# Performance work log

Measured on AMD Instinct MI355X. Metric: run time of the kernel, lower is better.

## Reference

```python
import jax, jax.numpy as jnp
import numpy as np

TEMPERATURE = 0.5


def setup_inputs() -> dict:
    key = jax.random.key(0)
    k1, k2 = jax.random.split(key)
    N, D = 4096, 512
    emb_i = jax.random.normal(k1, (N, D), dtype=jnp.float32)
    emb_j = jax.random.normal(k2, (N, D), dtype=jnp.float32)
    return {"emb_i": emb_i, "emb_j": emb_j}


def reference(emb_i, emb_j):
    # L2-normalize each embedding row (F.normalize, dim=1)
    z_i = emb_i / jnp.linalg.norm(emb_i, axis=1, keepdims=True)
    z_j = emb_j / jnp.linalg.norm(emb_j, axis=1, keepdims=True)
    reps = jnp.concatenate([z_i, z_j], axis=0)  # [2N, D]
    N = emb_i.shape[0]
    M = 2 * N
    # cosine similarity of normalized vectors == dot product -> [2N, 2N]
    sim = jnp.einsum('id,jd->ij', reps, reps) / TEMPERATURE
    # denominator: sum_k!=i exp(sim[i,k]); original multiplies by one-hot complement
    exp_sim = jnp.exp(sim)
    denom = jnp.sum(exp_sim, axis=1) - jnp.diagonal(exp_sim)  # [2N]
    log_denom = jnp.log(denom)
    # positive pairs: (k, k+N) and (k+N, k)
    idx = jnp.arange(N)
    pos_ij = sim[idx, idx + N]          # sim(k, k+N)/T
    pos_ji = sim[idx + N, idx]          # sim(k+N, k)/T
    loss = jnp.sum(-(pos_ij - log_denom[:N]) - (pos_ji - log_denom[N:]))
    return loss / (2.0 * N)
```

## Files before the change

kernel.cpp:

```cpp
#include <hip/hip_runtime.h>
#include <cstdint>
#include <cstddef>

constexpr int N_ROWS = 4096;
constexpr int D      = 512;
constexpr int M      = 8192;
constexpr int NTILE  = 64;
constexpr int NBLK   = NTILE * (NTILE + 1) / 2;
constexpr int BKB    = 64;
constexpr int LDSB   = 128 * BKB;

using f32x16 = __attribute__((ext_vector_type(16))) float;
using i32x4  = __attribute__((ext_vector_type(4))) int;
using i32x8  = __attribute__((ext_vector_type(8))) int;
using ul2    = __attribute__((ext_vector_type(2))) unsigned long;

#define ASYNC_CP16(gsrc, ldst)                                                      \
    __builtin_amdgcn_global_load_lds(                                               \
        (const __attribute__((address_space(1))) unsigned int*)(gsrc),              \
        (__attribute__((address_space(3))) unsigned int*)(ldst), 16, 0, 0)

#define SS_FP8(pk, accum)                                                           \
    do {                                                                            \
        float f0 = __builtin_amdgcn_cvt_f32_fp8((pk), 0);                           \
        float f1 = __builtin_amdgcn_cvt_f32_fp8((pk), 1);                           \
        float f2 = __builtin_amdgcn_cvt_f32_fp8((pk), 2);                           \
        float f3 = __builtin_amdgcn_cvt_f32_fp8((pk), 3);                           \
        (accum) += f0 * f0 + f1 * f1 + f2 * f2 + f3 * f3;                           \
    } while (0)

__global__ __launch_bounds__(256) void normpos_kernel(
    const float* __restrict__ emb_i, const float* __restrict__ emb_j,
    uint8_t* __restrict__ zb, float* __restrict__ diagss,
    float* __restrict__ pos)
{
    const int wave = threadIdx.x >> 6, lane = threadIdx.x & 63;
    const int k = blockIdx.x * 4 + wave;

    const float4* a = (const float4*)(emb_i + (size_t)k * D);
    const float4* b = (const float4*)(emb_j + (size_t)k * D);
    float4 a0 = a[lane * 2], a1 = a[lane * 2 + 1];
    float4 b0 = b[lane * 2], b1 = b[lane * 2 + 1];

    float ssi = a0.x*a0.x + a0.y*a0.y + a0.z*a0.z + a0.w*a0.w
              + a1.x*a1.x + a1.y*a1.y + a1.z*a1.z + a1.w*a1.w;
    float ssj = b0.x*b0.x + b0.y*b0.y + b0.z*b0.z + b0.w*b0.w
              + b1.x*b1.x + b1.y*b1.y + b1.z*b1.z + b1.w*b1.w;
    float dp  = a0.x*b0.x + a0.y*b0.y + a0.z*b0.z + a0.w*b0.w
              + a1.x*b1.x + a1.y*b1.y + a1.z*b1.z + a1.w*b1.w;
    #pragma unroll
    for (int off = 32; off; off >>= 1) {
        ssi += __shfl_xor(ssi, off, 64);
        ssj += __shfl_xor(ssj, off, 64);
        dp  += __shfl_xor(dp,  off, 64);
    }
    const float invi = rsqrtf(ssi), invj = rsqrtf(ssj);

    const float zi[8] = {a0.x*invi, a0.y*invi, a0.z*invi, a0.w*invi,
                         a1.x*invi, a1.y*invi, a1.z*invi, a1.w*invi};
    const float zj[8] = {b0.x*invj, b0.y*invj, b0.z*invj, b0.w*invj,
                         b1.x*invj, b1.y*invj, b1.z*invj, b1.w*invj};

    int pi0 = __builtin_amdgcn_cvt_pk_fp8_f32(zi[0], zi[1], 0, false);
    pi0     = __builtin_amdgcn_cvt_pk_fp8_f32(zi[2], zi[3], pi0, true);
    int pi1 = __builtin_amdgcn_cvt_pk_fp8_f32(zi[4], zi[5], 0, false);
    pi1     = __builtin_amdgcn_cvt_pk_fp8_f32(zi[6], zi[7], pi1, true);
    int pj0 = __builtin_amdgcn_cvt_pk_fp8_f32(zj[0], zj[1], 0, false);
    pj0     = __builtin_amdgcn_cvt_pk_fp8_f32(zj[2], zj[3], pj0, true);
    int pj1 = __builtin_amdgcn_cvt_pk_fp8_f32(zj[4], zj[5], 0, false);
    pj1     = __builtin_amdgcn_cvt_pk_fp8_f32(zj[6], zj[7], pj1, true);

    float dssi = 0.f, dssj = 0.f;
    SS_FP8(pi0, dssi);
    SS_FP8(pi1, dssi);
    SS_FP8(pj0, dssj);
    SS_FP8(pj1, dssj);

    const unsigned long long vi =
        ((unsigned long long)(unsigned)pi1 << 32) | (unsigned)pi0;
    const unsigned long long vj =
        ((unsigned long long)(unsigned)pj1 << 32) | (unsigned)pj0;
    *(unsigned long long*)(zb + (size_t)k * D + lane * 8)            = vi;
    *(unsigned long long*)(zb + (size_t)(k + N_ROWS) * D + lane * 8) = vj;

    #pragma unroll
    for (int off = 32; off; off >>= 1) {
        dssi += __shfl_xor(dssi, off, 64);
        dssj += __shfl_xor(dssj, off, 64);
    }
    if (lane == 0) {
        diagss[k]          = dssi;
        diagss[k + N_ROWS] = dssj;
        pos[k]             = 2.0f * dp * invi * invj;
    }
}

__global__ __launch_bounds__(256, 4) void simgemm_kernel(
    const uint8_t* __restrict__ zb, float* __restrict__ partials)
{
    __shared__ ul2 AsV[2 * LDSB / 16];
    __shared__ ul2 BsV[2 * LDSB / 16];
    __shared__ float rp[4][64];
    __shared__ float cp4[4][64];
    uint8_t* As = (uint8_t*)AsV;
    uint8_t* Bs = (uint8_t*)BsV;

    const int tid  = threadIdx.x;
    const int wave = tid >> 6, lane = tid & 63;
    const int l31  = lane & 31, half = lane >> 5;

    const int t = blockIdx.x;
    int bi = (int)((129.0f - sqrtf(129.0f * 129.0f - 8.0f * (float)t)) * 0.5f);
    while (bi > 0 && bi * (129 - bi) / 2 > t) --bi;
    while ((bi + 1) * (129 - (bi + 1)) / 2 <= t) ++bi;
    const int bj = bi + (t - bi * (129 - bi) / 2);
    const bool diag = (bi == bj);

    const int wrow = (wave >> 1) * 64, wcol = (wave & 1) * 64;

    const int srow = wave * 32 + (lane >> 2);
    const int scol = ((lane & 3) ^ ((lane >> 3) & 3)) * 16;
    const uint8_t* gA = zb + (size_t)(bi * 128 + srow) * D + scol;
    const uint8_t* gB = zb + (size_t)(bj * 128 + srow) * D + scol;
    uint8_t* lA = As + wave * 32 * BKB;
    uint8_t* lB = Bs + wave * 32 * BKB;

    ASYNC_CP16(gA,            lA);
    ASYNC_CP16(gA + 16 * D,   lA + 16 * BKB);
    ASYNC_CP16(gB,            lB);
    ASYNC_CP16(gB + 16 * D,   lB + 16 * BKB);

    f32x16 acc[2][2] = {};
    const int c0b = ((2 * half) ^ ((l31 >> 1) & 3)) * 16;

    for (int it = 0; it < D / BKB; ++it) {
        __syncthreads();

        if (it + 1 < D / BKB) {
            const int kc  = (it + 1) * BKB;
            const int off = ((it + 1) & 1) * LDSB;
            ASYNC_CP16(gA + kc,          lA + off);
            ASYNC_CP16(gA + kc + 16 * D, lA + off + 16 * BKB);
            ASYNC_CP16(gB + kc,          lB + off);
            ASYNC_CP16(gB + kc + 16 * D, lB + off + 16 * BKB);
        }

        const int cb = (it & 1) * LDSB;
        i32x8 af[2], bf[2];
        #pragma unroll
        for (int f = 0; f < 2; ++f) {
            const uint8_t* pa = As + cb + (size_t)(wrow + f * 32 + l31) * BKB;
            i32x4 alo = *(const i32x4*)(pa + c0b);
            i32x4 ahi = *(const i32x4*)(pa + (c0b ^ 16));
            af[f] = __builtin_shufflevector(alo, ahi, 0, 1, 2, 3, 4, 5, 6, 7);
            const uint8_t* pb = Bs + cb + (size_t)(wcol + f * 32 + l31) * BKB;
            i32x4 blo = *(const i32x4*)(pb + c0b);
            i32x4 bhi = *(const i32x4*)(pb + (c0b ^ 16));
            bf[f] = __builtin_shufflevector(blo, bhi, 0, 1, 2, 3, 4, 5, 6, 7);
        }
        #pragma unroll
        for (int i = 0; i < 2; ++i)
            #pragma unroll
            for (int j = 0; j < 2; ++j)
                acc[i][j] = __builtin_amdgcn_mfma_scale_f32_32x32x64_f8f6f4(
                    af[i], bf[j], acc[i][j], 0, 0,
                    0, 0x7f7f7f7f, 0, 0x7f7f7f7f);
    }

    float rowp[2][16] = {};
    #pragma unroll
    for (int j = 0; j < 2; ++j) {
        float cpj = 0.f;
        #pragma unroll
        for (int i = 0; i < 2; ++i)
            #pragma unroll
            for (int r = 0; r < 16; ++r) {
                float e = __expf(2.0f * acc[i][j][r]);
                rowp[i][r] += e;
                cpj += e;
            }
        if (!diag) {
            cpj += __shfl_xor(cpj, 32, 64);
            if (half == 0) cp4[wave][j * 32 + l31] = cpj;
        }
    }
    #pragma unroll
    for (int i = 0; i < 2; ++i)
        #pragma unroll
        for (int r = 0; r < 16; ++r) {
            float e = rowp[i][r];
            e += __shfl_xor(e, 1, 64);
            e += __shfl_xor(e, 2, 64);
            e += __shfl_xor(e, 4, 64);
            e += __shfl_xor(e, 8, 64);
            e += __shfl_xor(e, 16, 64);
            if (l31 == 0)
                rp[wave][i * 32 + (r & 3) + 8 * (r >> 2) + 4 * half] = e;
        }
    __syncthreads();

    float* pA = partials + (size_t)(bi * NTILE + bj) * 128;
    float* pB = partials + (size_t)(bj * NTILE + bi) * 128;
    if (tid < 128) {
        const int h = tid >> 6, rr = tid & 63;
        pA[tid] = rp[h * 2][rr] + rp[h * 2 + 1][rr];
    } else if (!diag) {
        const int c = tid - 128, h = c >> 6, cc = c & 63;
        pB[c] = cp4[h][cc] + cp4[h + 2][cc];
    }
}

__global__ __launch_bounds__(256) void rowfin_kernel(
    const float* __restrict__ partials, const float* __restrict__ diagss,
    const float* __restrict__ pos, float* __restrict__ lgpart)
{
    const int r  = blockIdx.x;
    const int ri = threadIdx.x & 127;
    const int ch = threadIdx.x >> 7;
    const float* base = partials + (size_t)r * NTILE * 128 + ri;
    float s = 0.f;
    #pragma unroll
    for (int c = 0; c < 32; ++c)
        s += base[(size_t)(ch * 32 + c) * 128];
    __shared__ float half1[128];
    __shared__ float red[4];
    if (ch == 1) half1[ri] = s;
    __syncthreads();
    float lg = 0.f;
    if (ch == 0) {
        float rs = s + half1[ri];
        int row = r * 128 + ri;
        lg = __logf(rs - __expf(2.0f * diagss[row]));
    }
    if (threadIdx.x < 64)
        lg -= 2.0f * pos[r * 64 + threadIdx.x];
    #pragma unroll
    for (int off = 32; off; off >>= 1) lg += __shfl_xor(lg, off, 64);
    const int wave = threadIdx.x >> 6, lane = threadIdx.x & 63;
    if (lane == 0) red[wave] = lg;
    __syncthreads();
    if (threadIdx.x == 0) lgpart[r] = red[0] + red[1] + red[2] + red[3];
}

__global__ __launch_bounds__(64) void loss_kernel(
    const float* __restrict__ lgpart, float* __restrict__ out)
{
    float local = lgpart[threadIdx.x];
    #pragma unroll
    for (int off = 32; off; off >>= 1) local += __shfl_xor(local, off, 64);
    if (threadIdx.x == 0) out[0] = local * (1.0f / 8192.0f);
}

extern "C" void kernel_launch(void* const* d_in, const int* in_sizes, int n_in,
                              void* d_out, int out_size, void* d_ws, size_t ws_size,
                              hipStream_t stream)
{
    const float* emb_i = (const float*)d_in[0];
    const float* emb_j = (const float*)d_in[1];

    uint8_t* zb = (uint8_t*)d_ws;
    float* partials = (float*)((char*)d_ws + (size_t)M * D);
    float* diagss   = partials + (size_t)NTILE * NTILE * 128;
    float* pos      = diagss + M;
    float* lgpart   = pos + N_ROWS;
    float* out      = (float*)d_out;

    normpos_kernel<<<N_ROWS / 4, 256, 0, stream>>>(emb_i, emb_j, zb, diagss, pos);
    simgemm_kernel<<<NBLK, 256, 0, stream>>>(zb, partials);
    rowfin_kernel<<<NTILE, 256, 0, stream>>>(partials, diagss, pos, lgpart);
    loss_kernel<<<1, 64, 0, stream>>>(lgpart, out);
}
```

Before: 116.5 us.

## Store FP8 embeddings in MFMA fragment layout and load directly to registers

The normalize kernel now writes the FP8 normalized embeddings in a tiled layout that matches the MFMA 32x32x64 operand fragments. The GEMM kernel can then skip the LDS staging and barriers and load fragments straight from global memory into registers, double-buffering them across K steps. This removes the LDS traffic and the per-iteration __syncthreads. The cost is that each wave fetches its own operands from global/L2 without sharing through LDS, and the extra fragment registers lower occupancy to 3 blocks per SIMD.

New measurement: 108.5 us. 6.9% less time.

```diff
diff --git a/kernel.cpp b/kernel.cpp
--- a/kernel.cpp
+++ b/kernel.cpp
@@ -7,18 +7,11 @@
 constexpr int M      = 8192;
 constexpr int NTILE  = 64;
 constexpr int NBLK   = NTILE * (NTILE + 1) / 2;
-constexpr int BKB    = 64;
-constexpr int LDSB   = 128 * BKB;
+constexpr int NKT    = 8;
 
 using f32x16 = __attribute__((ext_vector_type(16))) float;
 using i32x4  = __attribute__((ext_vector_type(4))) int;
 using i32x8  = __attribute__((ext_vector_type(8))) int;
-using ul2    = __attribute__((ext_vector_type(2))) unsigned long;
-
-#define ASYNC_CP16(gsrc, ldst)                                                      \
-    __builtin_amdgcn_global_load_lds(                                               \
-        (const __attribute__((address_space(1))) unsigned int*)(gsrc),              \
-        (__attribute__((address_space(3))) unsigned int*)(ldst), 16, 0, 0)
 
 #define SS_FP8(pk, accum)                                                           \
     do {                                                                            \
@@ -29,6 +22,7 @@
         (accum) += f0 * f0 + f1 * f1 + f2 * f2 + f3 * f3;                           \
     } while (0)
 
+
 __global__ __launch_bounds__(256) void normpos_kernel(
     const float* __restrict__ emb_i, const float* __restrict__ emb_j,
     uint8_t* __restrict__ zb, float* __restrict__ diagss,
@@ -76,12 +70,16 @@
     SS_FP8(pj0, dssj);
     SS_FP8(pj1, dssj);
 
+    const size_t off8 = (size_t)((k >> 5) * 8 + (lane >> 3)) * 2048
+                      + (size_t)(((lane >> 1) & 1)) * 1024
+                      + (size_t)(((k & 31) * 2 + ((lane >> 2) & 1))) * 16
+                      + (size_t)((lane & 1)) * 8;
     const unsigned long long vi =
         ((unsigned long long)(unsigned)pi1 << 32) | (unsigned)pi0;
     const unsigned long long vj =
         ((unsigned long long)(unsigned)pj1 << 32) | (unsigned)pj0;
-    *(unsigned long long*)(zb + (size_t)k * D + lane * 8)            = vi;
-    *(unsigned long long*)(zb + (size_t)(k + N_ROWS) * D + lane * 8) = vj;
+    *(unsigned long long*)(zb + off8)                       = vi;
+    *(unsigned long long*)(zb + off8 + (size_t)N_ROWS * D)  = vj;
 
     #pragma unroll
     for (int off = 32; off; off >>= 1) {
@@ -95,15 +93,11 @@
     }
 }
 
-__global__ __launch_bounds__(256, 4) void simgemm_kernel(
+__global__ __launch_bounds__(256, 3) void simgemm_kernel(
     const uint8_t* __restrict__ zb, float* __restrict__ partials)
 {
-    __shared__ ul2 AsV[2 * LDSB / 16];
-    __shared__ ul2 BsV[2 * LDSB / 16];
     __shared__ float rp[4][64];
     __shared__ float cp4[4][64];
-    uint8_t* As = (uint8_t*)AsV;
-    uint8_t* Bs = (uint8_t*)BsV;
 
     const int tid  = threadIdx.x;
     const int wave = tid >> 6, lane = tid & 63;
@@ -116,55 +110,46 @@
     const int bj = bi + (t - bi * (129 - bi) / 2);
     const bool diag = (bi == bj);
 
-    const int wrow = (wave >> 1) * 64, wcol = (wave & 1) * 64;
-
-    const int srow = wave * 32 + (lane >> 2);
-    const int scol = ((lane & 3) ^ ((lane >> 3) & 3)) * 16;
-    const uint8_t* gA = zb + (size_t)(bi * 128 + srow) * D + scol;
-    const uint8_t* gB = zb + (size_t)(bj * 128 + srow) * D + scol;
-    uint8_t* lA = As + wave * 32 * BKB;
-    uint8_t* lB = Bs + wave * 32 * BKB;
-
-    ASYNC_CP16(gA,            lA);
-    ASYNC_CP16(gA + 16 * D,   lA + 16 * BKB);
-    ASYNC_CP16(gB,            lB);
-    ASYNC_CP16(gB + 16 * D,   lB + 16 * BKB);
+    const int wr = wave >> 1, wc = wave & 1;
+
+    const int lofs = ((l31 << 1) | half) * 16;
+    const uint8_t* baseA0 = zb + (size_t)(bi * 4 + wr * 2    ) * 8 * 2048 + lofs;
+    const uint8_t* baseA1 = zb + (size_t)(bi * 4 + wr * 2 + 1) * 8 * 2048 + lofs;
+    const uint8_t* baseB0 = zb + (size_t)(bj * 4 + wc * 2    ) * 8 * 2048 + lofs;
+    const uint8_t* baseB1 = zb + (size_t)(bj * 4 + wc * 2 + 1) * 8 * 2048 + lofs;
+
+#define LDFRAG(DST, BP, IT)                                                         \
+    do {                                                                            \
+        i32x4 _lo = *(const i32x4*)((BP) + (size_t)(IT) * 2048);                    \
+        i32x4 _hi = *(const i32x4*)((BP) + (size_t)(IT) * 2048 + 1024);             \
+        DST = __builtin_shufflevector(_lo, _hi, 0, 1, 2, 3, 4, 5, 6, 7);            \
+    } while (0)
 
     f32x16 acc[2][2] = {};
-    const int c0b = ((2 * half) ^ ((l31 >> 1) & 3)) * 16;
-
-    for (int it = 0; it < D / BKB; ++it) {
-        __syncthreads();
-
-        if (it + 1 < D / BKB) {
-            const int kc  = (it + 1) * BKB;
-            const int off = ((it + 1) & 1) * LDSB;
-            ASYNC_CP16(gA + kc,          lA + off);
-            ASYNC_CP16(gA + kc + 16 * D, lA + off + 16 * BKB);
-            ASYNC_CP16(gB + kc,          lB + off);
-            ASYNC_CP16(gB + kc + 16 * D, lB + off + 16 * BKB);
+    i32x8 fA0[2], fA1[2], fB0[2], fB1[2];
+
+    LDFRAG(fA0[0], baseA0, 0);
+    LDFRAG(fA1[0], baseA1, 0);
+    LDFRAG(fB0[0], baseB0, 0);
+    LDFRAG(fB1[0], baseB1, 0);
+
+    #pragma unroll
+    for (int it = 0; it < NKT; ++it) {
+        const int cur = it & 1, nxt = cur ^ 1;
+        if (it + 1 < NKT) {
+            LDFRAG(fA0[nxt], baseA0, it + 1);
+            LDFRAG(fA1[nxt], baseA1, it + 1);
+            LDFRAG(fB0[nxt], baseB0, it + 1);
+            LDFRAG(fB1[nxt], baseB1, it + 1);
         }
-
-        const int cb = (it & 1) * LDSB;
-        i32x8 af[2], bf[2];
-        #pragma unroll
-        for (int f = 0; f < 2; ++f) {
-            const uint8_t* pa = As + cb + (size_t)(wrow + f * 32 + l31) * BKB;
-            i32x4 alo = *(const i32x4*)(pa + c0b);
-            i32x4 ahi = *(const i32x4*)(pa + (c0b ^ 16));
-            af[f] = __builtin_shufflevector(alo, ahi, 0, 1, 2, 3, 4, 5, 6, 7);
-            const uint8_t* pb = Bs + cb + (size_t)(wcol + f * 32 + l31) * BKB;
-            i32x4 blo = *(const i32x4*)(pb + c0b);
-            i32x4 bhi = *(const i32x4*)(pb + (c0b ^ 16));
-            bf[f] = __builtin_shufflevector(blo, bhi, 0, 1, 2, 3, 4, 5, 6, 7);
-        }
-        #pragma unroll
-        for (int i = 0; i < 2; ++i)
-            #pragma unroll
-            for (int j = 0; j < 2; ++j)
-                acc[i][j] = __builtin_amdgcn_mfma_scale_f32_32x32x64_f8f6f4(
-                    af[i], bf[j], acc[i][j], 0, 0,
-                    0, 0x7f7f7f7f, 0, 0x7f7f7f7f);
+        acc[0][0] = __builtin_amdgcn_mfma_scale_f32_32x32x64_f8f6f4(
+            fA0[cur], fB0[cur], acc[0][0], 0, 0, 0, 0x7f7f7f7f, 0, 0x7f7f7f7f);
+        acc[0][1] = __builtin_amdgcn_mfma_scale_f32_32x32x64_f8f6f4(
+            fA0[cur], fB1[cur], acc[0][1], 0, 0, 0, 0x7f7f7f7f, 0, 0x7f7f7f7f);
+        acc[1][0] = __builtin_amdgcn_mfma_scale_f32_32x32x64_f8f6f4(
+            fA1[cur], fB0[cur], acc[1][0], 0, 0, 0, 0x7f7f7f7f, 0, 0x7f7f7f7f);
+        acc[1][1] = __builtin_amdgcn_mfma_scale_f32_32x32x64_f8f6f4(
+            fA1[cur], fB1[cur], acc[1][1], 0, 0, 0, 0x7f7f7f7f, 0, 0x7f7f7f7f);
     }
 
     float rowp[2][16] = {};
```
